# Optimization experiments

Hardware: AMD Instinct MI355X
Metric: run time of the kernel (lower is better)

The kernel has to match this reference:

```python
import jax, jax.numpy as jnp
import numpy as np

LSH_NUM_PROJS = 7
BLOCK_SIZE = 256
SAMPLE_SIZE = 256
B, H, N, D = 2, 16, 8192, 64


def _gray_perm(num_projs):
    # Gray-code ordering so adjacent hash buckets differ by 1 bit (AngularLSH.perm)
    a = np.array([0, 1], dtype=np.int32)
    for _ in range(num_projs - 1):
        a = np.concatenate([a, a[::-1] + a.shape[0]])
    return a

_PERM = jnp.asarray(_gray_perm(LSH_NUM_PROJS))
_ENC = 2 ** jnp.arange(LSH_NUM_PROJS, dtype=jnp.int32)


def lsh_hash(x, proj_dir):
    # x: [b,h,n,d], proj_dir: [1,1,d,r] -> bucket ids [b,h,n]
    proj = jnp.einsum('...nd,...dr->...nr', x, proj_dir)
    bits = (proj > 0).astype(jnp.int32)
    return _PERM[(bits * _ENC).sum(-1)]


def gather_seq(x, idx):
    # x: [b,h,n,d], idx: [b,h,s] -> [b,h,s,d]
    return jnp.take_along_axis(x, idx[..., None], axis=2)


def setup_inputs() -> dict:
    key = jax.random.key(0)
    kq, kk, kv, kp, ks = jax.random.split(key, 5)
    query = jax.random.normal(kq, (B, H, N, D), dtype=jnp.float32)
    key_t = jax.random.normal(kk, (B, H, N, D), dtype=jnp.float32)
    value = jax.random.normal(kv, (B, H, N, D), dtype=jnp.float32)
    proj_dir = jax.random.normal(kp, (1, 1, D, LSH_NUM_PROJS), dtype=jnp.float32)
    # uniform sampling WITHOUT replacement per (b,h), like torch.multinomial
    skeys = jax.random.split(ks, B * H)
    sampled_set = jax.vmap(lambda k: jax.random.permutation(k, N)[:SAMPLE_SIZE])(skeys)
    sampled_set = sampled_set.reshape(B, H, SAMPLE_SIZE).astype(jnp.int32)
    return {'query': query, 'key': key_t, 'value': value,
            'proj_dir': proj_dir, 'sampled_set': sampled_set}


def reference(query, key, value, proj_dir, sampled_set):
    b, h, n, d = query.shape
    scale = d ** -0.5
    neg_min = jnp.finfo(query.dtype).min

    # ---- 1. LSH-sort queries and keys (stable sort on bucket ids) ----
    q_idx = jnp.argsort(lsh_hash(query, proj_dir), axis=2, stable=True)
    k_idx = jnp.argsort(lsh_hash(key, proj_dir), axis=2, stable=True)
    q_idx_inv = jnp.argsort(q_idx, axis=2, stable=True)
    q_s = gather_seq(query, q_idx)
    k_s = gather_seq(key, k_idx)
    v_s = gather_seq(value, k_idx)

    # ---- 2. block-diagonal exact attention on sorted order ----
    nb = n // BLOCK_SIZE               # n divisible by block_size (8192/256=32)
    qbs = n // nb                       # query_block_size == 256 here
    qb = q_s.reshape(b, h, nb, qbs, d)
    kb = k_s.reshape(b, h, nb, BLOCK_SIZE, d)
    vb = v_s.reshape(b, h, nb, BLOCK_SIZE, d)
    qk = jnp.einsum('bhnqd,bhnkd->bhnqk', qb, kb) * scale
    lse_blk = jax.nn.logsumexp(qk, axis=-1, keepdims=True)
    attn_blk = jnp.einsum('bhnqk,bhnkd->bhnqd', jnp.exp(qk - lse_blk), vb)
    attn_blk = attn_blk.reshape(b, h, n, d)
    lse_blk = lse_blk.reshape(b, h, n, 1)

    # ---- 3. sampled-column residual attention ----
    k_sub = gather_seq(k_s, sampled_set)   # [b,h,S,d]
    v_sub = gather_seq(v_s, sampled_set)
    row_blk = (jnp.arange(n) // qbs)[None, None, :, None]            # [1,1,n,1]
    col_blk = (sampled_set // BLOCK_SIZE)[:, :, None, :]             # [b,h,1,S]
    in_block = row_blk == col_blk                                    # [b,h,n,S]
    sampled_cnt = SAMPLE_SIZE - in_block.sum(-1, keepdims=True).astype(query.dtype)
    bias = in_block.astype(query.dtype) * neg_min                    # mask double-counted cols
    qk_r = jnp.einsum('bhnd,bhsd->bhns', q_s, k_sub) * scale + bias
    lse_r = jax.nn.logsumexp(qk_r, axis=-1, keepdims=True)
    attn_r = jnp.einsum('bhns,bhsd->bhnd', jnp.exp(qk_r - lse_r), v_sub)
    # approximate_unsampled: rescale sampled mass to stand in for all
    # (n - block_size) out-of-block columns
    lse_r = lse_r + jnp.log((n - BLOCK_SIZE) / sampled_cnt)

    # ---- 4. combine the two attention estimates (add_self_attentions) ----
    lse = jnp.logaddexp(lse_blk, lse_r)
    c = jnp.exp(lse_blk - lse)
    attn = c * attn_blk + (1.0 - c) * attn_r

    # ---- 5. un-sort rows back to original query order ----
    attn = gather_seq(attn, q_idx_inv)
    return attn
```

## Files before the change

kernel.cpp:

```cpp
#include <hip/hip_runtime.h>
#include <math.h>

#define BH    32
#define NSEQ  8192
#define DDIM  64
#define NPROJ 7
#define BLK   256
#define NB    32
#define PITCH 72
#define PPITCH 40
#define LOG2E 1.44269504f
#define SC2   0.180336881f

typedef _Float16 v8h __attribute__((ext_vector_type(8)));
typedef _Float16 v4h __attribute__((ext_vector_type(4)));
typedef float    v4f __attribute__((ext_vector_type(4)));

__global__ __launch_bounds__(256) void hash_kernel(
        const float* __restrict__ query,
        const float* __restrict__ key,
        const float* __restrict__ proj,
        int* __restrict__ buckets)
{
    const float* x = (blockIdx.y == 0) ? query : key;
    const int t = threadIdx.x;
    const int row = blockIdx.x * 256 + t;

    __shared__ double pdd[64 * NPROJ];
    for (int i = t; i < 64 * NPROJ; i += 256) pdd[i] = (double)proj[i];
    __syncthreads();

    const float4* rp = (const float4*)(x + (size_t)row * DDIM);
    double acc[NPROJ];
    #pragma unroll
    for (int r = 0; r < NPROJ; ++r) acc[r] = 0.0;

    #pragma unroll
    for (int i = 0; i < 16; ++i) {
        float4 v = rp[i];
        float e[4] = {v.x, v.y, v.z, v.w};
        #pragma unroll
        for (int c = 0; c < 4; ++c) {
            double xv = (double)e[c];
            const int d = i * 4 + c;
            #pragma unroll
            for (int r = 0; r < NPROJ; ++r)
                acc[r] += xv * pdd[d * NPROJ + r];
        }
    }
    int code = 0;
    #pragma unroll
    for (int r = 0; r < NPROJ; ++r)
        if (acc[r] > 0.0) code |= (1 << r);
    buckets[(size_t)blockIdx.y * (BH * NSEQ) + row] = code ^ (code >> 1);
}

#define SCNT 258
__global__ __launch_bounds__(256) void sort_kernel(
        const int* __restrict__ buckets,
        int* __restrict__ q_idx,
        int* __restrict__ k_idx)
{
    const int bh = blockIdx.x;
    const int t = threadIdx.x;
    const int lane = t & 63, w = t >> 6;
    const int* b = buckets + (size_t)blockIdx.y * (BH * NSEQ) + (size_t)bh * NSEQ;
    int* out = ((blockIdx.y == 0) ? q_idx : k_idx) + (size_t)bh * NSEQ;

    __shared__ unsigned short cnt[128 * SCNT];
    __shared__ unsigned int partial[256];
    __shared__ unsigned int wsum[4];

    unsigned int* cz = (unsigned int*)cnt;
    for (int i = t; i < 128 * SCNT / 2; i += 256) cz[i] = 0;

    int4 rv[8];
    const int4* b4 = (const int4*)b;
    #pragma unroll
    for (int s = 0; s < 8; ++s) rv[s] = b4[t * 8 + s];
    __syncthreads();

    #pragma unroll
    for (int s = 0; s < 8; ++s) {
        cnt[rv[s].x * SCNT + t]++;
        cnt[rv[s].y * SCNT + t]++;
        cnt[rv[s].z * SCNT + t]++;
        cnt[rv[s].w * SCNT + t]++;
    }
    __syncthreads();

    const int v0 = t >> 1, tt0 = (t & 1) * 128;
    {
        unsigned int s = 0;
        for (int j = 0; j < 128; ++j) s += cnt[v0 * SCNT + tt0 + j];
        partial[t] = s;
    }
    __syncthreads();

    unsigned int chunkoff;
    {
        unsigned int x = partial[t], own = x;
        #pragma unroll
        for (int d = 1; d < 64; d <<= 1) {
            unsigned int y = __shfl_up(x, d);
            if (lane >= d) x += y;
        }
        if (lane == 63) wsum[w] = x;
        __syncthreads();
        unsigned int wb0 = 0;
        if (w == 1) wb0 = wsum[0];
        else if (w == 2) wb0 = wsum[0] + wsum[1];
        else if (w == 3) wb0 = wsum[0] + wsum[1] + wsum[2];
        chunkoff = x - own + wb0;
    }

    {
        unsigned int s = chunkoff;
        for (int j = 0; j < 128; ++j) {
            unsigned short c = cnt[v0 * SCNT + tt0 + j];
            cnt[v0 * SCNT + tt0 + j] = (unsigned short)s;
            s += c;
        }
    }
    __syncthreads();

    const int i0 = t * 32;
    #pragma unroll
    for (int s = 0; s < 8; ++s) {
        int4 q = rv[s];
        int j4 = i0 + s * 4;
        { unsigned short p = cnt[q.x * SCNT + t]++; out[p] = j4 + 0; }
        { unsigned short p = cnt[q.y * SCNT + t]++; out[p] = j4 + 1; }
        { unsigned short p = cnt[q.z * SCNT + t]++; out[p] = j4 + 2; }
        { unsigned short p = cnt[q.w * SCNT + t]++; out[p] = j4 + 3; }
    }
}

__global__ __launch_bounds__(256, 3) void attn_kernel(
        const float* __restrict__ query,
        const float* __restrict__ key,
        const float* __restrict__ value,
        const int* __restrict__ sampled,
        const int* __restrict__ q_idx,
        const int* __restrict__ k_idx,
        float* __restrict__ outp)
{
    const int qb = blockIdx.x;
    const int bh = blockIdx.y;
    const int t  = threadIdx.x;
    const int w    = t >> 6;
    const int lane = t & 63;
    const int quad = lane >> 4;
    const int nrow = lane & 15;

    __shared__ __align__(16) unsigned char smem[38912];
    _Float16* Kc = (_Float16*)smem;
    _Float16* Vt = (_Float16*)(smem + 9216);
    _Float16* Pb = (_Float16*)(smem + 18432);
    _Float16* Ob = (_Float16*)smem;
    __shared__ int s_row[512];
    __shared__ __align__(16) float lb[512];
    __shared__ int s_qi[256];
    __shared__ int wb[4];

    const size_t bhN = (size_t)bh * NSEQ;

    {
        s_qi[t] = q_idx[bhN + qb * BLK + t];
        s_row[t] = k_idx[bhN + qb * BLK + t];
        int ss = sampled[bh * BLK + t];
        s_row[256 + t] = k_idx[bhN + ss];
        int sb = ss >> 8;
        unsigned long long mk = __ballot(sb == qb);
        if (lane == 0) wb[w] = __popcll(mk);
        __syncthreads();
        int cnt_in = wb[0] + wb[1] + wb[2] + wb[3];
        float J = __logf((float)(NSEQ - BLK) / (float)(BLK - cnt_in));
        lb[t] = -6.0f * LOG2E;
        lb[256 + t] = (sb == qb) ? -3.0e4f : (J - 6.0f) * LOG2E;
    }

    v8h qf[4][2];
    #pragma unroll
    for (int ni = 0; ni < 4; ++ni) {
        int qi = s_qi[w * 64 + ni * 16 + nrow];
        const float* qp = query + (bhN + (size_t)qi) * DDIM;
        #pragma unroll
        for (int k2 = 0; k2 < 2; ++k2) {
            const float4* q4 = (const float4*)(qp + k2 * 32 + quad * 8);
            float4 a = q4[0], bvec = q4[1];
            v8h h;
            h[0]=(_Float16)a.x; h[1]=(_Float16)a.y; h[2]=(_Float16)a.z; h[3]=(_Float16)a.w;
            h[4]=(_Float16)bvec.x; h[5]=(_Float16)bvec.y; h[6]=(_Float16)bvec.z; h[7]=(_Float16)bvec.w;
            qf[ni][k2] = h;
        }
    }

    v4f Oacc[4][4];
    v4f lacc[4];
    #pragma unroll
    for (int ni = 0; ni < 4; ++ni) {
        lacc[ni] = (v4f){0.f, 0.f, 0.f, 0.f};
        #pragma unroll
        for (int mi2 = 0; mi2 < 4; ++mi2) Oacc[mi2][ni] = (v4f){0.f, 0.f, 0.f, 0.f};
    }
    const v8h ones = {(_Float16)1, (_Float16)1, (_Float16)1, (_Float16)1,
                      (_Float16)1, (_Float16)1, (_Float16)1, (_Float16)1};
    _Float16* Pw = Pb + w * 64 * PPITCH;

    for (int ch = 0; ch < 8; ++ch) {
        __syncthreads();
        {
            int r = t >> 2, seg = t & 3;
            int kr = s_row[ch * 64 + r];
            const float4* kp = (const float4*)(key + (bhN + (size_t)kr) * DDIM + seg * 16);
            float4 a0 = kp[0], a1 = kp[1], a2 = kp[2], a3 = kp[3];
            v8h h0, h1;
            h0[0]=(_Float16)a0.x; h0[1]=(_Float16)a0.y; h0[2]=(_Float16)a0.z; h0[3]=(_Float16)a0.w;
            h0[4]=(_Float16)a1.x; h0[5]=(_Float16)a1.y; h0[6]=(_Float16)a1.z; h0[7]=(_Float16)a1.w;
            h1[0]=(_Float16)a2.x; h1[1]=(_Float16)a2.y; h1[2]=(_Float16)a2.z; h1[3]=(_Float16)a2.w;
            h1[4]=(_Float16)a3.x; h1[5]=(_Float16)a3.y; h1[6]=(_Float16)a3.z; h1[7]=(_Float16)a3.w;
            *(v8h*)&Kc[r * PITCH + seg * 16] = h0;
            *(v8h*)&Kc[r * PITCH + seg * 16 + 8] = h1;
        }
        {
            int kq = t & 15, dg = t >> 4;
            float la[4][4];
            #pragma unroll
            for (int c = 0; c < 4; ++c) {
                int vr = s_row[ch * 64 + kq * 4 + c];
                float4 v = *(const float4*)(value + (bhN + (size_t)vr) * DDIM + dg * 4);
                la[c][0] = v.x; la[c][1] = v.y; la[c][2] = v.z; la[c][3] = v.w;
            }
            #pragma unroll
            for (int dd = 0; dd < 4; ++dd) {
                v4h h;
                h[0]=(_Float16)la[0][dd]; h[1]=(_Float16)la[1][dd];
                h[2]=(_Float16)la[2][dd]; h[3]=(_Float16)la[3][dd];
                *(v4h*)&Vt[(dg * 4 + dd) * PITCH + kq * 4] = h;
            }
        }
        __syncthreads();

        #pragma unroll
        for (int ks = 0; ks < 2; ++ks) {
            #pragma unroll
            for (int mi = 0; mi < 2; ++mi) {
                v4f bb = *(const v4f*)&lb[ch * 64 + ks * 32 + mi * 16 + quad * 4];
                const int krow = ks * 32 + mi * 16 + nrow;
                v8h ka0 = *(const v8h*)&Kc[krow * PITCH + quad * 8];
                v8h ka1 = *(const v8h*)&Kc[krow * PITCH + 32 + quad * 8];
                #pragma unroll
                for (int ni = 0; ni < 4; ++ni) {
                    v4f S = (v4f){0.f, 0.f, 0.f, 0.f};
                    S = __builtin_amdgcn_mfma_f32_16x16x32_f16(ka0, qf[ni][0], S, 0, 0, 0);
                    S = __builtin_amdgcn_mfma_f32_16x16x32_f16(ka1, qf[ni][1], S, 0, 0, 0);
                    v4h ph;
                    #pragma unroll
                    for (int r = 0; r < 4; ++r)
                        ph[r] = (_Float16)__builtin_amdgcn_exp2f(fmaf(S[r], SC2, bb[r]));
                    *(v4h*)&Pw[(ni * 16 + nrow) * PPITCH + mi * 16 + quad * 4] = ph;
                }
            }
            v8h pbv[4];
            #pragma unroll
            for (int ni = 0; ni < 4; ++ni) {
                pbv[ni] = *(const v8h*)&Pw[(ni * 16 + nrow) * PPITCH + quad * 8];
                lacc[ni] = __builtin_amdgcn_mfma_f32_16x16x32_f16(ones, pbv[ni], lacc[ni], 0, 0, 0);
            }
            #pragma unroll
            for (int mi2 = 0; mi2 < 4; ++mi2) {
                v8h va = *(const v8h*)&Vt[(mi2 * 16 + nrow) * PITCH + ks * 32 + quad * 8];
                #pragma unroll
                for (int ni = 0; ni < 4; ++ni)
                    Oacc[mi2][ni] = __builtin_amdgcn_mfma_f32_16x16x32_f16(va, pbv[ni], Oacc[mi2][ni], 0, 0, 0);
            }
        }
    }

    __syncthreads();
    #pragma unroll
    for (int ni = 0; ni < 4; ++ni) {
        float inv = 1.0f / lacc[ni][0];
        #pragma unroll
        for (int mi2 = 0; mi2 < 4; ++mi2) {
            v4h h;
            #pragma unroll
            for (int r = 0; r < 4; ++r)
                h[r] = (_Float16)(Oacc[mi2][ni][r] * inv);
            *(v4h*)&Ob[(w * 64 + ni * 16 + nrow) * PITCH + mi2 * 16 + quad * 4] = h;
        }
    }
    __syncthreads();

    #pragma unroll
    for (int p = 0; p < 4; ++p) {
        int row = p * 64 + (t >> 2);
        int seg = t & 3;
        const _Float16* src = &Ob[row * PITCH + seg * 16];
        v8h x0 = *(const v8h*)src;
        v8h x1 = *(const v8h*)(src + 8);
        int qi = s_qi[row];
        float4* op = (float4*)(outp + (bhN + (size_t)qi) * DDIM + seg * 16);
        op[0] = make_float4((float)x0[0], (float)x0[1], (float)x0[2], (float)x0[3]);
        op[1] = make_float4((float)x0[4], (float)x0[5], (float)x0[6], (float)x0[7]);
        op[2] = make_float4((float)x1[0], (float)x1[1], (float)x1[2], (float)x1[3]);
        op[3] = make_float4((float)x1[4], (float)x1[5], (float)x1[6], (float)x1[7]);
    }
}

extern "C" void kernel_launch(void* const* d_in, const int* in_sizes, int n_in,
                              void* d_out, int out_size, void* d_ws, size_t ws_size,
                              hipStream_t stream) {
    (void)in_sizes; (void)n_in; (void)out_size; (void)ws_size;
    const float* query = (const float*)d_in[0];
    const float* key   = (const float*)d_in[1];
    const float* value = (const float*)d_in[2];
    const float* proj  = (const float*)d_in[3];
    const int* sampled = (const int*)d_in[4];
    float* out = (float*)d_out;

    int* buckets = (int*)d_ws;
    int* q_idx   = buckets + 2 * BH * NSEQ;
    int* k_idx   = q_idx + BH * NSEQ;

    hash_kernel<<<dim3(BH * NSEQ / 256, 2), 256, 0, stream>>>(query, key, proj, buckets);
    sort_kernel<<<dim3(BH, 2), 256, 0, stream>>>(buckets, q_idx, k_idx);
    attn_kernel<<<dim3(NB, BH), 256, 0, stream>>>(query, key, value, sampled,
                                                  q_idx, k_idx, out);
}
```

Baseline: 300.1 us.

## Prefetch next K/V chunk into registers and compute row sums with shuffles

Global loads of the next chunk's gathered key and value rows are issued into registers before the current chunk's MFMA work, so memory latency overlaps compute instead of stalling after each barrier. The row-sum normalizer, previously computed with an extra MFMA against a ones vector, is now accumulated per lane in scalar adds and reduced with cross-lane shuffles at the end. s_setprio is also raised around the PV MFMA block. The prefetch holds 32 extra float registers live across the loop, which may lower occupancy.

```diff
diff --git a/kernel.cpp b/kernel.cpp
--- a/kernel.cpp
+++ b/kernel.cpp
@@ -180,6 +180,29 @@
         lb[256 + t] = (sb == qb) ? -3.0e4f : (J - 6.0f) * LOG2E;
     }
 
+    const int kr_r = t >> 2, kr_seg = t & 3;
+    const int vs_kq = t & 15, vs_dg = t >> 4;
+
+    float4 kreg0, kreg1, kreg2, kreg3;
+    float4 vreg0, vreg1, vreg2, vreg3;
+
+    #define ISSUE_LOADS(ch_) do {                                              \
+        int krow_ = s_row[(ch_) * 64 + kr_r];                                  \
+        const float4* kp_ = (const float4*)(key + (bhN + (size_t)krow_) * DDIM \
+                                            + kr_seg * 16);                    \
+        kreg0 = kp_[0]; kreg1 = kp_[1]; kreg2 = kp_[2]; kreg3 = kp_[3];        \
+        int vr0_ = s_row[(ch_) * 64 + vs_kq * 4 + 0];                          \
+        int vr1_ = s_row[(ch_) * 64 + vs_kq * 4 + 1];                          \
+        int vr2_ = s_row[(ch_) * 64 + vs_kq * 4 + 2];                          \
+        int vr3_ = s_row[(ch_) * 64 + vs_kq * 4 + 3];                          \
+        vreg0 = *(const float4*)(value + (bhN + (size_t)vr0_) * DDIM + vs_dg * 4); \
+        vreg1 = *(const float4*)(value + (bhN + (size_t)vr1_) * DDIM + vs_dg * 4); \
+        vreg2 = *(const float4*)(value + (bhN + (size_t)vr2_) * DDIM + vs_dg * 4); \
+        vreg3 = *(const float4*)(value + (bhN + (size_t)vr3_) * DDIM + vs_dg * 4); \
+    } while (0)
+
+    ISSUE_LOADS(0);
+
     v8h qf[4][2];
     #pragma unroll
     for (int ni = 0; ni < 4; ++ni) {
@@ -197,49 +220,39 @@
     }
 
     v4f Oacc[4][4];
-    v4f lacc[4];
+    float l_part[4];
     #pragma unroll
     for (int ni = 0; ni < 4; ++ni) {
-        lacc[ni] = (v4f){0.f, 0.f, 0.f, 0.f};
+        l_part[ni] = 0.f;
         #pragma unroll
         for (int mi2 = 0; mi2 < 4; ++mi2) Oacc[mi2][ni] = (v4f){0.f, 0.f, 0.f, 0.f};
     }
-    const v8h ones = {(_Float16)1, (_Float16)1, (_Float16)1, (_Float16)1,
-                      (_Float16)1, (_Float16)1, (_Float16)1, (_Float16)1};
     _Float16* Pw = Pb + w * 64 * PPITCH;
 
+    #pragma unroll 1
     for (int ch = 0; ch < 8; ++ch) {
         __syncthreads();
         {
-            int r = t >> 2, seg = t & 3;
-            int kr = s_row[ch * 64 + r];
-            const float4* kp = (const float4*)(key + (bhN + (size_t)kr) * DDIM + seg * 16);
-            float4 a0 = kp[0], a1 = kp[1], a2 = kp[2], a3 = kp[3];
             v8h h0, h1;
-            h0[0]=(_Float16)a0.x; h0[1]=(_Float16)a0.y; h0[2]=(_Float16)a0.z; h0[3]=(_Float16)a0.w;
-            h0[4]=(_Float16)a1.x; h0[5]=(_Float16)a1.y; h0[6]=(_Float16)a1.z; h0[7]=(_Float16)a1.w;
-            h1[0]=(_Float16)a2.x; h1[1]=(_Float16)a2.y; h1[2]=(_Float16)a2.z; h1[3]=(_Float16)a2.w;
-            h1[4]=(_Float16)a3.x; h1[5]=(_Float16)a3.y; h1[6]=(_Float16)a3.z; h1[7]=(_Float16)a3.w;
-            *(v8h*)&Kc[r * PITCH + seg * 16] = h0;
-            *(v8h*)&Kc[r * PITCH + seg * 16 + 8] = h1;
+            h0[0]=(_Float16)kreg0.x; h0[1]=(_Float16)kreg0.y; h0[2]=(_Float16)kreg0.z; h0[3]=(_Float16)kreg0.w;
+            h0[4]=(_Float16)kreg1.x; h0[5]=(_Float16)kreg1.y; h0[6]=(_Float16)kreg1.z; h0[7]=(_Float16)kreg1.w;
+            h1[0]=(_Float16)kreg2.x; h1[1]=(_Float16)kreg2.y; h1[2]=(_Float16)kreg2.z; h1[3]=(_Float16)kreg2.w;
+            h1[4]=(_Float16)kreg3.x; h1[5]=(_Float16)kreg3.y; h1[6]=(_Float16)kreg3.z; h1[7]=(_Float16)kreg3.w;
+            *(v8h*)&Kc[kr_r * PITCH + kr_seg * 16] = h0;
+            *(v8h*)&Kc[kr_r * PITCH + kr_seg * 16 + 8] = h1;
         }
         {
-            int kq = t & 15, dg = t >> 4;
-            float la[4][4];
-            #pragma unroll
-            for (int c = 0; c < 4; ++c) {
-                int vr = s_row[ch * 64 + kq * 4 + c];
-                float4 v = *(const float4*)(value + (bhN + (size_t)vr) * DDIM + dg * 4);
-                la[c][0] = v.x; la[c][1] = v.y; la[c][2] = v.z; la[c][3] = v.w;
-            }
-            #pragma unroll
-            for (int dd = 0; dd < 4; ++dd) {
-                v4h h;
-                h[0]=(_Float16)la[0][dd]; h[1]=(_Float16)la[1][dd];
-                h[2]=(_Float16)la[2][dd]; h[3]=(_Float16)la[3][dd];
-                *(v4h*)&Vt[(dg * 4 + dd) * PITCH + kq * 4] = h;
-            }
-        }
+            v4h h0, h1, h2, h3;
+            h0[0]=(_Float16)vreg0.x; h0[1]=(_Float16)vreg1.x; h0[2]=(_Float16)vreg2.x; h0[3]=(_Float16)vreg3.x;
+            h1[0]=(_Float16)vreg0.y; h1[1]=(_Float16)vreg1.y; h1[2]=(_Float16)vreg2.y; h1[3]=(_Float16)vreg3.y;
+            h2[0]=(_Float16)vreg0.z; h2[1]=(_Float16)vreg1.z; h2[2]=(_Float16)vreg2.z; h2[3]=(_Float16)vreg3.z;
+            h3[0]=(_Float16)vreg0.w; h3[1]=(_Float16)vreg1.w; h3[2]=(_Float16)vreg2.w; h3[3]=(_Float16)vreg3.w;
+            *(v4h*)&Vt[(vs_dg * 4 + 0) * PITCH + vs_kq * 4] = h0;
+            *(v4h*)&Vt[(vs_dg * 4 + 1) * PITCH + vs_kq * 4] = h1;
+            *(v4h*)&Vt[(vs_dg * 4 + 2) * PITCH + vs_kq * 4] = h2;
+            *(v4h*)&Vt[(vs_dg * 4 + 3) * PITCH + vs_kq * 4] = h3;
+        }
+        if (ch < 7) ISSUE_LOADS(ch + 1);
         __syncthreads();
 
         #pragma unroll
@@ -259,15 +272,16 @@
                     #pragma unroll
                     for (int r = 0; r < 4; ++r)
                         ph[r] = (_Float16)__builtin_amdgcn_exp2f(fmaf(S[r], SC2, bb[r]));
+                    l_part[ni] += ((float)ph[0] + (float)ph[1])
+                                + ((float)ph[2] + (float)ph[3]);
                     *(v4h*)&Pw[(ni * 16 + nrow) * PPITCH + mi * 16 + quad * 4] = ph;
                 }
             }
             v8h pbv[4];
             #pragma unroll
-            for (int ni = 0; ni < 4; ++ni) {
+            for (int ni = 0; ni < 4; ++ni)
                 pbv[ni] = *(const v8h*)&Pw[(ni * 16 + nrow) * PPITCH + quad * 8];
-                lacc[ni] = __builtin_amdgcn_mfma_f32_16x16x32_f16(ones, pbv[ni], lacc[ni], 0, 0, 0);
-            }
+            __builtin_amdgcn_s_setprio(1);
             #pragma unroll
             for (int mi2 = 0; mi2 < 4; ++mi2) {
                 v8h va = *(const v8h*)&Vt[(mi2 * 16 + nrow) * PITCH + ks * 32 + quad * 8];
@@ -275,13 +289,17 @@
                 for (int ni = 0; ni < 4; ++ni)
                     Oacc[mi2][ni] = __builtin_amdgcn_mfma_f32_16x16x32_f16(va, pbv[ni], Oacc[mi2][ni], 0, 0, 0);
             }
+            __builtin_amdgcn_s_setprio(0);
         }
     }
 
     __syncthreads();
     #pragma unroll
     for (int ni = 0; ni < 4; ++ni) {
-        float inv = 1.0f / lacc[ni][0];
+        float l = l_part[ni];
+        l += __shfl_xor(l, 16);
+        l += __shfl_xor(l, 32);
+        float inv = 1.0f / l;
         #pragma unroll
         for (int mi2 = 0; mi2 < 4; ++mi2) {
             v4h h;
```

Result: slower. 350.8 us (+16.9%).
